# Kernel tuning notes

Measured on AMD Instinct MI355X. Metric: run time of the kernel, lower is better.

## Reference

```python
import jax, jax.numpy as jnp
import numpy as np

N = 100000   # nodes
E = 1600000  # edges
T = 4        # GCN layers
F = 48       # feature dim (16*3 from concat of x,h,q)


def setup_inputs() -> dict:
    key = jax.random.key(0)
    k0, k1, k2, k3, k4 = jax.random.split(key, 5)
    h = jax.random.normal(k0, (N, 16), jnp.float32)
    x = jax.random.normal(k1, (N, 16), jnp.float32)
    q = jax.random.normal(k2, (N, 16), jnp.float32)
    e = jax.random.randint(k3, (2, E), 0, N, dtype=jnp.int32)  # edge_index [src; dst]
    mask = jnp.ones((N,), jnp.bool_)
    # GCNConv params: lin weight [out,in] (glorot-ish), bias [out] (zeros init in PyG)
    W = jax.random.normal(k4, (T, F, F), jnp.float32) * (1.0 / np.sqrt(F))
    b = jnp.zeros((T, F), jnp.float32)
    return {"h": h, "e": e, "x": x, "q": q, "mask": mask, "W": W, "b": b}


def _gcn_layer(feat, src, dst, W_t, b_t):
    # PyG GCNConv with add_self_loops=True, normalize=True:
    # out[i] = sum_{j->i} (deg_i^-1/2 deg_j^-1/2) (W feat_j) + deg_i^-1 (W feat_i) + b
    xw = feat @ W_t.T  # [N, F]
    ones = jnp.ones(src.shape[0], xw.dtype)
    deg = jax.ops.segment_sum(ones, dst, num_segments=N) + 1.0  # +1 from self-loop
    dis = jax.lax.rsqrt(deg)  # deg >= 1 always
    norm = dis[src] * dis[dst]  # [E]
    agg = jax.ops.segment_sum(xw[src] * norm[:, None], dst, num_segments=N)
    agg = agg + xw * (dis * dis)[:, None]  # self-loop term
    return agg + b_t


def reference(h, e, x, q, mask, W, b):
    feat = jnp.concatenate([x, h, q], axis=-1)  # [N, 48] = inp_atom_i
    src, dst = e[0], e[1]
    out = feat
    # NOTE: original loop applies every layer to inp_atom_i (not chained);
    # only the last layer's output is returned. Reproduce that exactly.
    for t in range(T):
        out = _gcn_layer(feat, src, dst, W[t], b[t])
    return out
```

## Files before the change

kernel.cpp:

```cpp
#include <hip/hip_runtime.h>

#define FDIM 48
#define FV 12
#define CAPR 48
#define NXCD 8
#define EPB_A 2048
#define SCAN_T 256
#define SCAN_ITEMS 16
#define SCAN_CHUNK (SCAN_T * SCAN_ITEMS)


__global__ __launch_bounds__(256) void bin_kernel(const int* __restrict__ src,
                                                  const int* __restrict__ dst,
                                                  int* __restrict__ cur,
                                                  int* __restrict__ buckets,
                                                  int E, int rstep, int bcap) {
    __shared__ int lcnt[NXCD];
    __shared__ int lscan[NXCD];
    __shared__ int gbase[NXCD];
    __shared__ int stage[EPB_A];
    int tid = threadIdx.x;
    if (tid < NXCD) lcnt[tid] = 0;
    __syncthreads();

    int base = blockIdx.x * EPB_A + tid * 8;
    int rr[8], oo[8], vv[8];
    int nloc = 0;
    if (base + 8 <= E) {
        int4 d0 = *(const int4*)(dst + base);
        int4 d1 = *(const int4*)(dst + base + 4);
        int4 s0 = *(const int4*)(src + base);
        int4 s1 = *(const int4*)(src + base + 4);
        int ds[8] = {d0.x, d0.y, d0.z, d0.w, d1.x, d1.y, d1.z, d1.w};
        int ss[8] = {s0.x, s0.y, s0.z, s0.w, s1.x, s1.y, s1.z, s1.w};
#pragma unroll
        for (int k = 0; k < 8; ++k) {
            int r = ds[k] / rstep;
            rr[k] = r;
            vv[k] = ((ds[k] - r * rstep) << 17) | ss[k];
            oo[k] = atomicAdd(&lcnt[r], 1);
        }
        nloc = 8;
    } else {
#pragma unroll
        for (int k = 0; k < 8; ++k) {
            int i = base + k;
            if (i < E) {
                int d = dst[i];
                int r = d / rstep;
                rr[k] = r;
                vv[k] = ((d - r * rstep) << 17) | src[i];
                oo[k] = atomicAdd(&lcnt[r], 1);
                nloc = k + 1;
            }
        }
    }
    __syncthreads();
    if (tid == 0) {
        int run = 0;
        for (int r = 0; r < NXCD; ++r) { lscan[r] = run; run += lcnt[r]; }
    }
    if (tid < NXCD) gbase[tid] = atomicAdd(&cur[tid], lcnt[tid]);
    __syncthreads();
#pragma unroll
    for (int k = 0; k < 8; ++k)
        if (k < nloc) stage[lscan[rr[k]] + oo[k]] = vv[k];
    __syncthreads();
    for (int r = 0; r < NXCD; ++r) {
        int len = lcnt[r], gb = gbase[r], ls = lscan[r];
        int* bp = buckets + (size_t)r * bcap;
        for (int i = tid; i < len; i += 256) {
            int gi = gb + i;
            if (gi < bcap) bp[gi] = stage[ls + i];
        }
    }
}

__global__ __launch_bounds__(256) void fillB_kernel(const int* __restrict__ cur,
                                                    const int* __restrict__ buckets,
                                                    int* __restrict__ cnt,
                                                    int* __restrict__ csr,
                                                    int rstep, int bcap) {
    int r = blockIdx.x & (NXCD - 1);
    int chunk = blockIdx.x >> 3;
    int M = cur[r]; if (M > bcap) M = bcap;
    int lo = r * rstep;
    const int* bp = buckets + (size_t)r * bcap;
    int base = chunk * 1024 + threadIdx.x * 4;
    if (base >= M) return;
    if (base + 4 <= M) {
        int4 v4 = *(const int4*)(bp + base);
        int vs[4] = {v4.x, v4.y, v4.z, v4.w};
#pragma unroll
        for (int k = 0; k < 4; ++k) {
            int v = vs[k];
            int d = lo + (v >> 17);
            int s = v & 0x1FFFF;
            int p = atomicAdd(&cnt[d], 1);
            if (p < CAPR) csr[(size_t)d * CAPR + p] = s;
        }
    } else {
        for (int k = 0; k < 4 && base + k < M; ++k) {
            int v = bp[base + k];
            int d = lo + (v >> 17);
            int s = v & 0x1FFFF;
            int p = atomicAdd(&cnt[d], 1);
            if (p < CAPR) csr[(size_t)d * CAPR + p] = s;
        }
    }
}

__global__ __launch_bounds__(256) void gather3_kernel(const int* __restrict__ cnt,
                                                      const int* __restrict__ csr,
                                                      const float* __restrict__ y,
                                                      const float* __restrict__ dis,
                                                      const float* __restrict__ b3,
                                                      float* __restrict__ out, int N) {
    int g = blockIdx.x * 4 + (threadIdx.x >> 6);
    if (g >= N) return;
    int lane = threadIdx.x & 63;
    int grp = lane >> 4;
    int l = lane & 15;

    int m = cnt[g]; if (m > CAPR) m = CAPR;
    const int* row = csr + (size_t)g * CAPR;

    float a0 = 0.f, a1 = 0.f, a2 = 0.f;
    for (int j = grp; j < m; j += 4) {
        int s = row[j];
        const float* ys = y + (size_t)s * FDIM;
        a0 += ys[l]; a1 += ys[l + 16]; a2 += ys[l + 32];
    }
    a0 += __shfl_xor(a0, 16); a0 += __shfl_xor(a0, 32);
    a1 += __shfl_xor(a1, 16); a1 += __shfl_xor(a1, 32);
    a2 += __shfl_xor(a2, 16); a2 += __shfl_xor(a2, 32);

    if (grp == 0) {
        const float* yg = y + (size_t)g * FDIM;
        float di = dis[g];
        float* og = out + (size_t)g * FDIM;
        og[l]      = di * (a0 + yg[l])      + b3[l];
        og[l + 16] = di * (a1 + yg[l + 16]) + b3[l + 16];
        og[l + 32] = di * (a2 + yg[l + 32]) + b3[l + 32];
    }
}

__global__ __launch_bounds__(256) void xw_kernel(const float* __restrict__ x,
                                                 const float* __restrict__ h,
                                                 const float* __restrict__ q,
                                                 const float* __restrict__ W3,
                                                 const int* __restrict__ deg,
                                                 float* __restrict__ y,
                                                 float* __restrict__ dis, int N) {
    __shared__ float4 Ws4[FDIM * FV];
    for (int t = threadIdx.x; t < FDIM * FV; t += 256)
        Ws4[t] = ((const float4*)W3)[t];
    __syncthreads();

    int i = blockIdx.x * blockDim.x + threadIdx.x;
    if (i >= N) return;

    float feat[FDIM];
    const float4* x4 = (const float4*)(x + (size_t)i * 16);
    const float4* h4 = (const float4*)(h + (size_t)i * 16);
    const float4* q4 = (const float4*)(q + (size_t)i * 16);
#pragma unroll
    for (int c = 0; c < 4; ++c) {
        float4 v = x4[c];
        feat[4 * c + 0] = v.x; feat[4 * c + 1] = v.y;
        feat[4 * c + 2] = v.z; feat[4 * c + 3] = v.w;
    }
#pragma unroll
    for (int c = 0; c < 4; ++c) {
        float4 v = h4[c];
        feat[16 + 4 * c + 0] = v.x; feat[16 + 4 * c + 1] = v.y;
        feat[16 + 4 * c + 2] = v.z; feat[16 + 4 * c + 3] = v.w;
    }
#pragma unroll
    for (int c = 0; c < 4; ++c) {
        float4 v = q4[c];
        feat[32 + 4 * c + 0] = v.x; feat[32 + 4 * c + 1] = v.y;
        feat[32 + 4 * c + 2] = v.z; feat[32 + 4 * c + 3] = v.w;
    }

    float di = rsqrtf((float)deg[i] + 1.0f);
    dis[i] = di;

    float4* yrow = (float4*)(y + (size_t)i * FDIM);
#pragma unroll
    for (int oc = 0; oc < FV; ++oc) {
        float ax = 0.f, ay = 0.f, az = 0.f, aw = 0.f;
#pragma unroll
        for (int k4 = 0; k4 < FV; ++k4) {
            float f0 = feat[4 * k4 + 0], f1 = feat[4 * k4 + 1];
            float f2 = feat[4 * k4 + 2], f3 = feat[4 * k4 + 3];
            float4 w0 = Ws4[(4 * oc + 0) * FV + k4];
            float4 w1 = Ws4[(4 * oc + 1) * FV + k4];
            float4 w2 = Ws4[(4 * oc + 2) * FV + k4];
            float4 w3 = Ws4[(4 * oc + 3) * FV + k4];
            ax += f0 * w0.x + f1 * w0.y + f2 * w0.z + f3 * w0.w;
            ay += f0 * w1.x + f1 * w1.y + f2 * w1.z + f3 * w1.w;
            az += f0 * w2.x + f1 * w2.y + f2 * w2.z + f3 * w2.w;
            aw += f0 * w3.x + f1 * w3.y + f2 * w3.z + f3 * w3.w;
        }
        float4 r;
        r.x = ax * di; r.y = ay * di; r.z = az * di; r.w = aw * di;
        yrow[oc] = r;
    }
}

__global__ __launch_bounds__(256) void deg_kernel(const int* __restrict__ dst,
                                                  int* __restrict__ deg, int E) {
    int i = blockIdx.x * blockDim.x + threadIdx.x;
    if (i < E) atomicAdd(&deg[dst[i]], 1);
}

__global__ __launch_bounds__(SCAN_T) void scan_partial(const int* __restrict__ deg,
                                                       int* __restrict__ bsum, int N) {
    __shared__ int s[SCAN_T];
    int tid = threadIdx.x;
    int base = blockIdx.x * SCAN_CHUNK + tid * SCAN_ITEMS;
    int sum = 0;
    if (base + SCAN_ITEMS <= N) {
        const int4* p = (const int4*)(deg + base);
#pragma unroll
        for (int c = 0; c < SCAN_ITEMS / 4; ++c) {
            int4 v = p[c];
            sum += v.x + v.y + v.z + v.w;
        }
    } else {
        for (int k = 0; k < SCAN_ITEMS; ++k) {
            int i = base + k;
            if (i < N) sum += deg[i];
        }
    }
    s[tid] = sum;
    __syncthreads();
#pragma unroll
    for (int off = SCAN_T / 2; off > 0; off >>= 1) {
        if (tid < off) s[tid] += s[tid + off];
        __syncthreads();
    }
    if (tid == 0) bsum[blockIdx.x] = s[0];
}

__global__ __launch_bounds__(SCAN_T) void scan_bsum(int* __restrict__ bsum,
                                                    int* __restrict__ rowstart_N,
                                                    int nb) {
    __shared__ int s[SCAN_T];
    int tid = threadIdx.x;
    int v = (tid < nb) ? bsum[tid] : 0;
    s[tid] = v;
    __syncthreads();
#pragma unroll
    for (int off = 1; off < SCAN_T; off <<= 1) {
        int t = (tid >= off) ? s[tid - off] : 0;
        __syncthreads();
        s[tid] += t;
        __syncthreads();
    }
    if (tid < nb) bsum[tid] = s[tid] - v;
    if (tid == nb - 1) rowstart_N[0] = s[tid];
}

__global__ __launch_bounds__(SCAN_T) void scan_final(const int* __restrict__ deg,
                                                     const int* __restrict__ bsum,
                                                     int* __restrict__ rowstart,
                                                     int* __restrict__ cursor, int N) {
    __shared__ int s[SCAN_T];
    int tid = threadIdx.x;
    int base = blockIdx.x * SCAN_CHUNK + tid * SCAN_ITEMS;
    int vals[SCAN_ITEMS];
    int sum = 0;
    bool full = (base + SCAN_ITEMS <= N);
    if (full) {
        const int4* p = (const int4*)(deg + base);
#pragma unroll
        for (int c = 0; c < SCAN_ITEMS / 4; ++c) {
            int4 v = p[c];
            vals[4 * c + 0] = v.x; vals[4 * c + 1] = v.y;
            vals[4 * c + 2] = v.z; vals[4 * c + 3] = v.w;
            sum += v.x + v.y + v.z + v.w;
        }
    } else {
#pragma unroll
        for (int k = 0; k < SCAN_ITEMS; ++k) {
            int i = base + k;
            vals[k] = (i < N) ? deg[i] : 0;
            sum += vals[k];
        }
    }
    s[tid] = sum;
    __syncthreads();
#pragma unroll
    for (int off = 1; off < SCAN_T; off <<= 1) {
        int t = (tid >= off) ? s[tid - off] : 0;
        __syncthreads();
        s[tid] += t;
        __syncthreads();
    }
    int run = bsum[blockIdx.x] + s[tid] - sum;
    int pfx[SCAN_ITEMS];
#pragma unroll
    for (int k = 0; k < SCAN_ITEMS; ++k) {
        pfx[k] = run;
        run += vals[k];
    }
    if (full) {
        int4* rs4 = (int4*)(rowstart + base);
        int4* cu4 = (int4*)(cursor + base);
#pragma unroll
        for (int c = 0; c < SCAN_ITEMS / 4; ++c) {
            int4 v;
            v.x = pfx[4 * c + 0]; v.y = pfx[4 * c + 1];
            v.z = pfx[4 * c + 2]; v.w = pfx[4 * c + 3];
            rs4[c] = v;
            cu4[c] = v;
        }
    } else {
        for (int k = 0; k < SCAN_ITEMS; ++k) {
            int i = base + k;
            if (i < N) { rowstart[i] = pfx[k]; cursor[i] = pfx[k]; }
        }
    }
}

__global__ __launch_bounds__(256) void fill_kernel(const int* __restrict__ src,
                                                   const int* __restrict__ dst,
                                                   int* __restrict__ cursor,
                                                   int* __restrict__ csr_src, int E) {
    int i = blockIdx.x * blockDim.x + threadIdx.x;
    if (i >= E) return;
    int d = dst[i];
    int pos = atomicAdd(&cursor[d], 1);
    csr_src[pos] = src[i];
}

__global__ __launch_bounds__(256) void gather_kernel(const int* __restrict__ rowstart,
                                                     const int* __restrict__ csr_src,
                                                     const float* __restrict__ y,
                                                     const float* __restrict__ dis,
                                                     const float* __restrict__ b3,
                                                     float* __restrict__ out, int N) {
    int g = (blockIdx.x * blockDim.x + threadIdx.x) >> 4;
    int l = threadIdx.x & 15;
    if (g >= N) return;

    int beg = rowstart[g];
    int end = rowstart[g + 1];

    float a0 = 0.f, a1 = 0.f, a2 = 0.f;
    int j = beg;
    for (; j + 1 < end; j += 2) {
        int s0 = csr_src[j];
        int s1 = csr_src[j + 1];
        const float* y0 = y + (size_t)s0 * FDIM;
        const float* y1 = y + (size_t)s1 * FDIM;
        a0 += y0[l] + y1[l];
        a1 += y0[l + 16] + y1[l + 16];
        a2 += y0[l + 32] + y1[l + 32];
    }
    if (j < end) {
        int s0 = csr_src[j];
        const float* y0 = y + (size_t)s0 * FDIM;
        a0 += y0[l]; a1 += y0[l + 16]; a2 += y0[l + 32];
    }
    const float* yg = y + (size_t)g * FDIM;
    a0 += yg[l]; a1 += yg[l + 16]; a2 += yg[l + 32];

    float di = dis[g];
    float* og = out + (size_t)g * FDIM;
    og[l]      = di * a0 + b3[l];
    og[l + 16] = di * a1 + b3[l + 16];
    og[l + 32] = di * a2 + b3[l + 32];
}

extern "C" void kernel_launch(void* const* d_in, const int* in_sizes, int n_in,
                              void* d_out, int out_size, void* d_ws, size_t ws_size,
                              hipStream_t stream) {
    const float* h = (const float*)d_in[0];
    const int*   e = (const int*)d_in[1];
    const float* x = (const float*)d_in[2];
    const float* q = (const float*)d_in[3];
    const float* W = (const float*)d_in[5];
    const float* b = (const float*)d_in[6];

    int N = in_sizes[0] / 16;
    int E = in_sizes[1] / 2;
    size_t N4 = ((size_t)N + 3) & ~(size_t)3;

    const float* W3 = W + (size_t)3 * FDIM * FDIM;
    const float* b3 = b + (size_t)3 * FDIM;
    float* out = (float*)d_out;

    const int* src = e;
    const int* dst = e + E;

    int rstep = (N + NXCD - 1) / NXCD;
    int bcap = E / NXCD + 4096;

    size_t need_radix = (N4 * (FDIM + 2) + 16 + (size_t)N * CAPR) * 4;
    bool radix_ok = (ws_size >= need_radix) &&
                    ((size_t)NXCD * bcap <= N4 * FDIM) &&
                    (N <= (1 << 17)) && (rstep <= (1 << 14));

    if (radix_ok) {
        float* y   = (float*)d_ws;
        float* dis = y + N4 * FDIM;
        int*   cnt = (int*)(dis + N4);
        int*   cur = cnt + N4;
        int*   csr = cur + 16;
        int*   buckets = (int*)y;

        hipMemsetAsync(cnt, 0, (N4 + 16) * sizeof(int), stream);

        int nbA = (E + EPB_A - 1) / EPB_A;
        int nchB = (bcap + 1023) / 1024;
        bin_kernel<<<nbA, 256, 0, stream>>>(src, dst, cur, buckets, E, rstep, bcap);
        fillB_kernel<<<nchB * NXCD, 256, 0, stream>>>(cur, buckets, cnt, csr, rstep, bcap);
        xw_kernel<<<(N + 255) / 256, 256, 0, stream>>>(x, h, q, W3, cnt, y, dis, N);
        gather3_kernel<<<(N + 3) / 4, 256, 0, stream>>>(cnt, csr, y, dis, b3, out, N);
    } else {
        float* y        = (float*)d_ws;
        float* dis      = y + N4 * FDIM;
        int*   deg      = (int*)(dis + N4);
        int*   cursor   = deg + N4;
        int*   rowstart = cursor + N4;
        int*   bsum     = rowstart + N4 + 4;
        int*   csr_src  = bsum + 256;

        int nb = (N + SCAN_CHUNK - 1) / SCAN_CHUNK;

        hipMemsetAsync(deg, 0, (size_t)N * sizeof(int), stream);
        deg_kernel<<<(E + 255) / 256, 256, 0, stream>>>(dst, deg, E);
        scan_partial<<<nb, SCAN_T, 0, stream>>>(deg, bsum, N);
        scan_bsum<<<1, SCAN_T, 0, stream>>>(bsum, rowstart + N, nb);
        scan_final<<<nb, SCAN_T, 0, stream>>>(deg, bsum, rowstart, cursor, N);
        fill_kernel<<<(E + 255) / 256, 256, 0, stream>>>(src, dst, cursor, csr_src, E);
        xw_kernel<<<(N + 255) / 256, 256, 0, stream>>>(x, h, q, W3, deg, y, dis, N);
        gather_kernel<<<((size_t)N * 16 + 255) / 256, 256, 0, stream>>>(
            rowstart, csr_src, y, dis, b3, out, N);
    }
}
```

Measured before the change: 249.1 us.

## Build per-destination CSR in shared-memory windows and split xw across four threads

Replaces the global-atomic CSR fill with a window kernel. Each block rescans its whole destination bucket, keeps only edges whose destination falls in its 256-node window, and builds counts and rows with shared-memory atomics. It then writes the rows out as coalesced int4 stores and computes degrees and dis at the same time, which removes the count memset and the global atomics. The cost is that every bucket is read once per window, so the total bucket traffic is much larger. Separately, the xw stage now uses four threads per node, each computing three output float4 chunks, and the bin kernel's cursor counters are padded apart.

```diff
diff --git a/kernel.cpp b/kernel.cpp
--- a/kernel.cpp
+++ b/kernel.cpp
@@ -3,6 +3,7 @@
 #define FDIM 48
 #define FV 12
 #define CAPR 48
+#define SUBW 256
 #define NXCD 8
 #define EPB_A 2048
 #define SCAN_T 256
@@ -18,7 +19,7 @@
     __shared__ int lcnt[NXCD];
     __shared__ int lscan[NXCD];
     __shared__ int gbase[NXCD];
-    __shared__ int stage[EPB_A];
+    __shared__ __align__(16) int stage[EPB_A];
     int tid = threadIdx.x;
     if (tid < NXCD) lcnt[tid] = 0;
     __syncthreads();
@@ -60,7 +61,7 @@
         int run = 0;
         for (int r = 0; r < NXCD; ++r) { lscan[r] = run; run += lcnt[r]; }
     }
-    if (tid < NXCD) gbase[tid] = atomicAdd(&cur[tid], lcnt[tid]);
+    if (tid < NXCD) gbase[tid] = atomicAdd(&cur[tid * 16], lcnt[tid]);
     __syncthreads();
 #pragma unroll
     for (int k = 0; k < 8; ++k)
@@ -76,37 +77,126 @@
     }
 }
 
-__global__ __launch_bounds__(256) void fillB_kernel(const int* __restrict__ cur,
-                                                    const int* __restrict__ buckets,
-                                                    int* __restrict__ cnt,
-                                                    int* __restrict__ csr,
-                                                    int rstep, int bcap) {
+__global__ __launch_bounds__(256) void window_kernel(const int* __restrict__ cur,
+                                                     const int* __restrict__ buckets,
+                                                     int* __restrict__ cnt,
+                                                     float* __restrict__ dis,
+                                                     int* __restrict__ csr,
+                                                     int rstep, int bcap, int N) {
+    __shared__ int lcnt[SUBW];
+    __shared__ __align__(16) int lcsr[SUBW * CAPR];
     int r = blockIdx.x & (NXCD - 1);
-    int chunk = blockIdx.x >> 3;
-    int M = cur[r]; if (M > bcap) M = bcap;
-    int lo = r * rstep;
+    int w = blockIdx.x >> 3;
+    int tid = threadIdx.x;
+    lcnt[tid] = 0;
+    __syncthreads();
+
+    int M = cur[r * 16]; if (M > bcap) M = bcap;
     const int* bp = buckets + (size_t)r * bcap;
-    int base = chunk * 1024 + threadIdx.x * 4;
-    if (base >= M) return;
-    if (base + 4 <= M) {
-        int4 v4 = *(const int4*)(bp + base);
+
+    int nv = M >> 2;
+    for (int i = tid; i < nv; i += 256) {
+        int4 v4 = ((const int4*)bp)[i];
         int vs[4] = {v4.x, v4.y, v4.z, v4.w};
 #pragma unroll
         for (int k = 0; k < 4; ++k) {
             int v = vs[k];
-            int d = lo + (v >> 17);
-            int s = v & 0x1FFFF;
-            int p = atomicAdd(&cnt[d], 1);
-            if (p < CAPR) csr[(size_t)d * CAPR + p] = s;
-        }
-    } else {
-        for (int k = 0; k < 4 && base + k < M; ++k) {
-            int v = bp[base + k];
-            int d = lo + (v >> 17);
-            int s = v & 0x1FFFF;
-            int p = atomicAdd(&cnt[d], 1);
-            if (p < CAPR) csr[(size_t)d * CAPR + p] = s;
-        }
+            if ((v >> 25) == w) {
+                int dl = (v >> 17) & (SUBW - 1);
+                int p = atomicAdd(&lcnt[dl], 1);
+                if (p < CAPR) lcsr[dl * CAPR + p] = v & 0x1FFFF;
+            }
+        }
+    }
+    for (int i = (nv << 2) + tid; i < M; i += 256) {
+        int v = bp[i];
+        if ((v >> 25) == w) {
+            int dl = (v >> 17) & (SUBW - 1);
+            int p = atomicAdd(&lcnt[dl], 1);
+            if (p < CAPR) lcsr[dl * CAPR + p] = v & 0x1FFFF;
+        }
+    }
+    __syncthreads();
+
+    int nl = w * SUBW;
+    int g0 = r * rstep + nl;
+    int valid = rstep - nl; if (valid > SUBW) valid = SUBW;
+    if (valid > N - g0) valid = N - g0;
+    if (valid <= 0) return;
+
+    int tot4 = (valid * CAPR) >> 2;
+    int4* dst4 = (int4*)(csr + (size_t)g0 * CAPR);
+    const int4* src4 = (const int4*)lcsr;
+    for (int i = tid; i < tot4; i += 256) dst4[i] = src4[i];
+
+    if (tid < valid) {
+        int c = lcnt[tid];
+        cnt[g0 + tid] = c;
+        dis[g0 + tid] = rsqrtf((float)c + 1.0f);
+    }
+}
+
+__global__ __launch_bounds__(256) void xw4_kernel(const float* __restrict__ x,
+                                                  const float* __restrict__ h,
+                                                  const float* __restrict__ q,
+                                                  const float* __restrict__ W3,
+                                                  const float* __restrict__ dis,
+                                                  float* __restrict__ y, int N) {
+    __shared__ float4 Ws4[FDIM * FV];
+    for (int t = threadIdx.x; t < FDIM * FV; t += 256)
+        Ws4[t] = ((const float4*)W3)[t];
+    __syncthreads();
+
+    int gid = blockIdx.x * blockDim.x + threadIdx.x;
+    int i = gid >> 2;
+    if (i >= N) return;
+    int p = gid & 3;
+
+    float feat[FDIM];
+    const float4* x4 = (const float4*)(x + (size_t)i * 16);
+    const float4* h4 = (const float4*)(h + (size_t)i * 16);
+    const float4* q4 = (const float4*)(q + (size_t)i * 16);
+#pragma unroll
+    for (int c = 0; c < 4; ++c) {
+        float4 v = x4[c];
+        feat[4 * c + 0] = v.x; feat[4 * c + 1] = v.y;
+        feat[4 * c + 2] = v.z; feat[4 * c + 3] = v.w;
+    }
+#pragma unroll
+    for (int c = 0; c < 4; ++c) {
+        float4 v = h4[c];
+        feat[16 + 4 * c + 0] = v.x; feat[16 + 4 * c + 1] = v.y;
+        feat[16 + 4 * c + 2] = v.z; feat[16 + 4 * c + 3] = v.w;
+    }
+#pragma unroll
+    for (int c = 0; c < 4; ++c) {
+        float4 v = q4[c];
+        feat[32 + 4 * c + 0] = v.x; feat[32 + 4 * c + 1] = v.y;
+        feat[32 + 4 * c + 2] = v.z; feat[32 + 4 * c + 3] = v.w;
+    }
+
+    float di = dis[i];
+    float4* yrow = (float4*)(y + (size_t)i * FDIM);
+#pragma unroll
+    for (int j = 0; j < 3; ++j) {
+        int oc = 3 * p + j;
+        float ax = 0.f, ay = 0.f, az = 0.f, aw = 0.f;
+#pragma unroll
+        for (int k4 = 0; k4 < FV; ++k4) {
+            float f0 = feat[4 * k4 + 0], f1 = feat[4 * k4 + 1];
+            float f2 = feat[4 * k4 + 2], f3 = feat[4 * k4 + 3];
+            float4 w0 = Ws4[(4 * oc + 0) * FV + k4];
+            float4 w1 = Ws4[(4 * oc + 1) * FV + k4];
+            float4 w2 = Ws4[(4 * oc + 2) * FV + k4];
+            float4 w3 = Ws4[(4 * oc + 3) * FV + k4];
+            ax += f0 * w0.x + f1 * w0.y + f2 * w0.z + f3 * w0.w;
+            ay += f0 * w1.x + f1 * w1.y + f2 * w1.z + f3 * w1.w;
+            az += f0 * w2.x + f1 * w2.y + f2 * w2.z + f3 * w2.w;
+            aw += f0 * w3.x + f1 * w3.y + f2 * w3.z + f3 * w3.w;
+        }
+        float4 rr;
+        rr.x = ax * di; rr.y = ay * di; rr.z = az * di; rr.w = aw * di;
+        yrow[oc] = rr;
     }
 }
 
@@ -156,10 +246,8 @@
     for (int t = threadIdx.x; t < FDIM * FV; t += 256)
         Ws4[t] = ((const float4*)W3)[t];
     __syncthreads();
-
     int i = blockIdx.x * blockDim.x + threadIdx.x;
     if (i >= N) return;
-
     float feat[FDIM];
     const float4* x4 = (const float4*)(x + (size_t)i * 16);
     const float4* h4 = (const float4*)(h + (size_t)i * 16);
@@ -182,10 +270,8 @@
         feat[32 + 4 * c + 0] = v.x; feat[32 + 4 * c + 1] = v.y;
         feat[32 + 4 * c + 2] = v.z; feat[32 + 4 * c + 3] = v.w;
     }
-
     float di = rsqrtf((float)deg[i] + 1.0f);
     dis[i] = di;
-
     float4* yrow = (float4*)(y + (size_t)i * FDIM);
 #pragma unroll
     for (int oc = 0; oc < FV; ++oc) {
@@ -345,29 +431,16 @@
     int g = (blockIdx.x * blockDim.x + threadIdx.x) >> 4;
     int l = threadIdx.x & 15;
     if (g >= N) return;
-
     int beg = rowstart[g];
     int end = rowstart[g + 1];
-
     float a0 = 0.f, a1 = 0.f, a2 = 0.f;
-    int j = beg;
-    for (; j + 1 < end; j += 2) {
-        int s0 = csr_src[j];
-        int s1 = csr_src[j + 1];
-        const float* y0 = y + (size_t)s0 * FDIM;
-        const float* y1 = y + (size_t)s1 * FDIM;
-        a0 += y0[l] + y1[l];
-        a1 += y0[l + 16] + y1[l + 16];
-        a2 += y0[l + 32] + y1[l + 32];
-    }
-    if (j < end) {
+    for (int j = beg; j < end; ++j) {
         int s0 = csr_src[j];
         const float* y0 = y + (size_t)s0 * FDIM;
         a0 += y0[l]; a1 += y0[l + 16]; a2 += y0[l + 32];
     }
     const float* yg = y + (size_t)g * FDIM;
     a0 += yg[l]; a1 += yg[l + 16]; a2 += yg[l + 32];
-
     float di = dis[g];
     float* og = out + (size_t)g * FDIM;
     og[l]      = di * a0 + b3[l];
@@ -399,7 +472,7 @@
     int rstep = (N + NXCD - 1) / NXCD;
     int bcap = E / NXCD + 4096;
 
-    size_t need_radix = (N4 * (FDIM + 2) + 16 + (size_t)N * CAPR) * 4;
+    size_t need_radix = (N4 * (FDIM + 2) + 128 + N4 * CAPR) * 4;
     bool radix_ok = (ws_size >= need_radix) &&
                     ((size_t)NXCD * bcap <= N4 * FDIM) &&
                     (N <= (1 << 17)) && (rstep <= (1 << 14));
@@ -409,16 +482,17 @@
         float* dis = y + N4 * FDIM;
         int*   cnt = (int*)(dis + N4);
         int*   cur = cnt + N4;
-        int*   csr = cur + 16;
+        int*   csr = cur + 128;
         int*   buckets = (int*)y;
 
-        hipMemsetAsync(cnt, 0, (N4 + 16) * sizeof(int), stream);
+        hipMemsetAsync(cur, 0, 128 * sizeof(int), stream);
 
         int nbA = (E + EPB_A - 1) / EPB_A;
-        int nchB = (bcap + 1023) / 1024;
+        int nw = (rstep + SUBW - 1) / SUBW;
         bin_kernel<<<nbA, 256, 0, stream>>>(src, dst, cur, buckets, E, rstep, bcap);
-        fillB_kernel<<<nchB * NXCD, 256, 0, stream>>>(cur, buckets, cnt, csr, rstep, bcap);
-        xw_kernel<<<(N + 255) / 256, 256, 0, stream>>>(x, h, q, W3, cnt, y, dis, N);
+        window_kernel<<<nw * NXCD, 256, 0, stream>>>(cur, buckets, cnt, dis, csr,
+                                                     rstep, bcap, N);
+        xw4_kernel<<<((size_t)N * 4 + 255) / 256, 256, 0, stream>>>(x, h, q, W3, dis, y, N);
         gather3_kernel<<<(N + 3) / 4, 256, 0, stream>>>(cnt, csr, y, dis, b3, out, N);
     } else {
         float* y        = (float*)d_ws;
```

Result: slower. 284.9 us (+14.4%).
